# Performance work log

Hardware: AMD Instinct MI355X
Metric: run time of the kernel (lower is better)

## Reference

```python
import jax, jax.numpy as jnp
import numpy as np

B, SEQ = 1, 2048
HEADS, HEAD_DIM = 16, 64
HIDDEN = HEADS * HEAD_DIM          # 1024
EXP = 4
QKVP = HIDDEN * (3 + EXP)          # 7168
VP = HIDDEN * (1 + EXP)            # 5120
DEPTH = 12
EPS = 1e-5
NEG = -1e10


def _alibi_slopes(heads):
    def p2(n):
        start = 2.0 ** (-(2.0 ** (-(np.log2(n) - 3.0))))
        return [start * (start ** i) for i in range(n)]
    if np.log2(heads).is_integer():
        return p2(heads)
    c = 2 ** int(np.floor(np.log2(heads)))
    return p2(c) + p2(2 * c)[0::2][: heads - c]


def _ln(x, g, b):
    m = x.mean(-1, keepdims=True)
    v = ((x - m) ** 2).mean(-1, keepdims=True)
    return (x - m) / jnp.sqrt(v + EPS) * g + b


def setup_inputs():
    key = jax.random.key(0)
    ks = jax.random.split(key, 16)
    init_scale = 2.0 / (DEPTH ** 0.5)
    inp = {
        'x': jax.random.normal(ks[0], (B, SEQ, HIDDEN), jnp.float32),
        'accumulated_logits': 0.02 * jax.random.normal(ks[1], (B, 1, SEQ, SEQ), jnp.float32),
        'in_proj_w': (init_scale / HIDDEN ** 0.5) * jax.random.normal(ks[2], (QKVP, HIDDEN), jnp.float32),
        'out_proj_w': 0.02 * jax.random.normal(ks[3], (HIDDEN, VP), jnp.float32),
        'out_proj_b': 0.02 * jax.random.normal(ks[4], (HIDDEN,), jnp.float32),
        'in_ln_g': 1.0 + 0.02 * jax.random.normal(ks[5], (HIDDEN,), jnp.float32),
        'in_ln_b': 0.02 * jax.random.normal(ks[6], (HIDDEN,), jnp.float32),
        'q_ln_g': 1.0 + 0.02 * jax.random.normal(ks[7], (HIDDEN,), jnp.float32),
        'q_ln_b': 0.02 * jax.random.normal(ks[8], (HIDDEN,), jnp.float32),
        'k_ln_g': 1.0 + 0.02 * jax.random.normal(ks[9], (HIDDEN,), jnp.float32),
        'k_ln_b': 0.02 * jax.random.normal(ks[10], (HIDDEN,), jnp.float32),
        'mid_ln_g': 1.0 + 0.02 * jax.random.normal(ks[11], (HIDDEN * EXP,), jnp.float32),
        'mid_ln_b': 0.02 * jax.random.normal(ks[12], (HIDDEN * EXP,), jnp.float32),
        'out_ln_g': 1.0 + 0.02 * jax.random.normal(ks[13], (HIDDEN,), jnp.float32),
        'out_ln_b': 0.02 * jax.random.normal(ks[14], (HIDDEN,), jnp.float32),
    }
    return inp


def reference(x, accumulated_logits, in_proj_w, out_proj_w, out_proj_b,
              in_ln_g, in_ln_b, q_ln_g, q_ln_b, k_ln_g, k_ln_b,
              mid_ln_g, mid_ln_b, out_ln_g, out_ln_b):
    b, l, d = x.shape
    h = _ln(x, in_ln_g, in_ln_b)
    # Shift: first d//4 channels shifted forward by 1 token (zero-pad front)
    q4 = d // 4
    shifted = jnp.pad(h[:, :, :q4], ((0, 0), (1, 0), (0, 0)))[:, :l]
    h = jnp.concatenate([shifted, h[:, :, q4:]], axis=-1)
    # merged qkvp projection (no bias)
    h = h @ in_proj_w.T                                   # [b, l, qkvp]
    q, k, v, p = jnp.split(h, [HIDDEN, 2 * HIDDEN, 3 * HIDDEN], axis=-1)
    q = _ln(q, q_ln_g, q_ln_b)
    k = _ln(k, k_ln_g, k_ln_b)
    to_heads = lambda t: t.reshape(b, l, HEADS, HEAD_DIM).transpose(0, 2, 1, 3)
    qh, kh, vh = to_heads(q), to_heads(k), to_heads(v)    # [b, h, l, hd]
    logits = jnp.einsum('bhid,bhjd->bhij', qh, kh) * (HEAD_DIM ** -0.5)
    logit_residual = logits.mean(axis=1, keepdims=True)   # [b, 1, l, l]
    idx = jnp.arange(l)
    causal = jnp.where(idx[:, None] >= idx[None, :], 0.0, NEG).astype(x.dtype)
    slopes = jnp.asarray(_alibi_slopes(HEADS), jnp.float32)          # [h]
    alibi = idx.astype(jnp.float32)[None, :] * slopes[:, None]       # [h, j]
    logits = logits + accumulated_logits + alibi[None, :, None, :] + causal[None, None]
    a = jax.nn.softmax(logits, axis=-1)
    o = jnp.einsum('bhij,bhjd->bhid', a, vh)
    o = o.transpose(0, 2, 1, 3).reshape(b, l, HIDDEN)
    p = jax.nn.relu(_ln(p, mid_ln_g, mid_ln_b))
    out = jnp.concatenate([o, p], axis=-1) @ out_proj_w.T + out_proj_b
    out = _ln(out, out_ln_g, out_ln_b)
    return out, logit_residual
```

## Files before the change

### kernel.cpp

```cpp
#include <hip/hip_runtime.h>

#define SEQ 2048
#define HID 1024
#define NHEAD 16
#define HD 64
#define QKVPD 7168
#define VPD 5120
#define NEGV -1e10f

typedef __bf16 bf16;
typedef __attribute__((ext_vector_type(4))) __bf16 bf16x4;
typedef __attribute__((ext_vector_type(8))) __bf16 bf16x8;
typedef __attribute__((ext_vector_type(4))) float f32x4;

#define MFMA16(a, b, c) __builtin_amdgcn_mfma_f32_16x16x32_bf16((a), (b), (c), 0, 0, 0)

#define GLOAD_LDS16(g, l) __builtin_amdgcn_global_load_lds( \
    (const __attribute__((address_space(1))) void*)(g),     \
    (__attribute__((address_space(3))) void*)(l), 16, 0, 0)

__device__ __forceinline__ void reduce2(float& s, float& ss) {
#pragma unroll
  for (int mk = 32; mk >= 1; mk >>= 1) {
    s  += __shfl_xor(s, mk);
    ss += __shfl_xor(ss, mk);
  }
  __shared__ float rtmp[8];
  const int w = threadIdx.x >> 6;
  if ((threadIdx.x & 63) == 0) { rtmp[2 * w] = s; rtmp[2 * w + 1] = ss; }
  __syncthreads();
  s  = rtmp[0] + rtmp[2] + rtmp[4] + rtmp[6];
  ss = rtmp[1] + rtmp[3] + rtmp[5] + rtmp[7];
}

__global__ __launch_bounds__(256) void cvt_f32_bf16(const float* __restrict__ in,
                                                    bf16* __restrict__ out, int n4) {
  int i = blockIdx.x * 256 + threadIdx.x;
  if (i >= n4) return;
  float4 v = ((const float4*)in)[i];
  bf16x4 o = {(bf16)v.x, (bf16)v.y, (bf16)v.z, (bf16)v.w};
  ((bf16x4*)out)[i] = o;
}

__global__ __launch_bounds__(256) void ln_in_shift(const float* __restrict__ x,
                                                   const float* __restrict__ g,
                                                   const float* __restrict__ b,
                                                   bf16* __restrict__ h) {
  const int t = blockIdx.x, tid = threadIdx.x;
  float4 v = ((const float4*)(x + (size_t)t * HID))[tid];
  float s = v.x + v.y + v.z + v.w;
  float ss = v.x * v.x + v.y * v.y + v.z * v.z + v.w * v.w;
  reduce2(s, ss);
  float mean = s * (1.f / HID);
  float var = ss * (1.f / HID) - mean * mean;
  float rstd = rsqrtf(var + 1e-5f);
  int c0 = tid * 4;
  float4 gv = ((const float4*)g)[tid];
  float4 bv = ((const float4*)b)[tid];
  bf16x4 o;
  o[0] = (bf16)((v.x - mean) * rstd * gv.x + bv.x);
  o[1] = (bf16)((v.y - mean) * rstd * gv.y + bv.y);
  o[2] = (bf16)((v.z - mean) * rstd * gv.z + bv.z);
  o[3] = (bf16)((v.w - mean) * rstd * gv.w + bv.w);
  if (c0 >= 256) {
    *(bf16x4*)(h + (size_t)t * HID + c0) = o;
  } else {
    if (t + 1 < SEQ) *(bf16x4*)(h + (size_t)(t + 1) * HID + c0) = o;
    if (t == 0) {
      bf16x4 z = {(bf16)0.f, (bf16)0.f, (bf16)0.f, (bf16)0.f};
      *(bf16x4*)(h + c0) = z;
    }
  }
}

__global__ __launch_bounds__(256) void ln_qk(const bf16* __restrict__ qkvp,
                                             const float* __restrict__ gq, const float* __restrict__ bq,
                                             const float* __restrict__ gk, const float* __restrict__ bk,
                                             bf16* __restrict__ qo, bf16* __restrict__ ko) {
  const int t = blockIdx.x, z = blockIdx.y, tid = threadIdx.x;
  const bf16* in = qkvp + (size_t)t * QKVPD + z * HID;
  bf16* out = (z ? ko : qo) + (size_t)t * HID;
  const float* g = z ? gk : gq;
  const float* bb = z ? bk : bq;
  int c0 = tid * 4;
  bf16x4 iv = *(const bf16x4*)(in + c0);
  float f0 = (float)iv[0], f1 = (float)iv[1], f2 = (float)iv[2], f3 = (float)iv[3];
  float s = f0 + f1 + f2 + f3;
  float ss = f0 * f0 + f1 * f1 + f2 * f2 + f3 * f3;
  reduce2(s, ss);
  float mean = s * (1.f / HID);
  float var = ss * (1.f / HID) - mean * mean;
  float rstd = rsqrtf(var + 1e-5f);
  float4 gv = ((const float4*)g)[tid];
  float4 bv = ((const float4*)bb)[tid];
  bf16x4 o;
  o[0] = (bf16)((f0 - mean) * rstd * gv.x + bv.x);
  o[1] = (bf16)((f1 - mean) * rstd * gv.y + bv.y);
  o[2] = (bf16)((f2 - mean) * rstd * gv.z + bv.z);
  o[3] = (bf16)((f3 - mean) * rstd * gv.w + bv.w);
  *(bf16x4*)(out + c0) = o;
}

__global__ __launch_bounds__(256) void ln_mid(const bf16* __restrict__ qkvp,
                                              const float* __restrict__ g,
                                              const float* __restrict__ b,
                                              bf16* __restrict__ op) {
  const int t = blockIdx.x, tid = threadIdx.x;
  const bf16* in = qkvp + (size_t)t * QKVPD + 3 * HID;
  int c0 = tid * 16;
  bf16x8 a = *(const bf16x8*)(in + c0);
  bf16x8 a2 = *(const bf16x8*)(in + c0 + 8);
  float fv[16];
#pragma unroll
  for (int e = 0; e < 8; ++e) { fv[e] = (float)a[e]; fv[8 + e] = (float)a2[e]; }
  float s = 0.f, ss = 0.f;
#pragma unroll
  for (int e = 0; e < 16; ++e) { s += fv[e]; ss += fv[e] * fv[e]; }
  reduce2(s, ss);
  const float D = 4.f * HID;
  float mean = s / D;
  float var = ss / D - mean * mean;
  float rstd = rsqrtf(var + 1e-5f);
  bf16x8 o1, o2;
#pragma unroll
  for (int q = 0; q < 4; ++q) {
    float4 gv = ((const float4*)g)[tid * 4 + q];
    float4 bv = ((const float4*)b)[tid * 4 + q];
    float r0 = fmaxf(0.f, (fv[q * 4 + 0] - mean) * rstd * gv.x + bv.x);
    float r1 = fmaxf(0.f, (fv[q * 4 + 1] - mean) * rstd * gv.y + bv.y);
    float r2 = fmaxf(0.f, (fv[q * 4 + 2] - mean) * rstd * gv.z + bv.z);
    float r3 = fmaxf(0.f, (fv[q * 4 + 3] - mean) * rstd * gv.w + bv.w);
    if (q < 2) {
      o1[q * 4 + 0] = (bf16)r0; o1[q * 4 + 1] = (bf16)r1;
      o1[q * 4 + 2] = (bf16)r2; o1[q * 4 + 3] = (bf16)r3;
    } else {
      o2[(q - 2) * 4 + 0] = (bf16)r0; o2[(q - 2) * 4 + 1] = (bf16)r1;
      o2[(q - 2) * 4 + 2] = (bf16)r2; o2[(q - 2) * 4 + 3] = (bf16)r3;
    }
  }
  bf16* dst = op + (size_t)t * VPD + HID + c0;
  *(bf16x8*)dst = o1;
  *(bf16x8*)(dst + 8) = o2;
}

__global__ __launch_bounds__(256) void ln_out(const float* __restrict__ cp0,
                                              const float* __restrict__ cp1,
                                              const float* __restrict__ bias,
                                              const float* __restrict__ g,
                                              const float* __restrict__ b,
                                              float* __restrict__ outp) {
  const int t = blockIdx.x, tid = threadIdx.x;
  float4 v  = ((const float4*)(cp0 + (size_t)t * HID))[tid];
  float4 v1 = ((const float4*)(cp1 + (size_t)t * HID))[tid];
  float4 bi = ((const float4*)bias)[tid];
  v.x += v1.x + bi.x; v.y += v1.y + bi.y; v.z += v1.z + bi.z; v.w += v1.w + bi.w;
  float s = v.x + v.y + v.z + v.w;
  float ss = v.x * v.x + v.y * v.y + v.z * v.z + v.w * v.w;
  reduce2(s, ss);
  float mean = s * (1.f / HID);
  float var = ss * (1.f / HID) - mean * mean;
  float rstd = rsqrtf(var + 1e-5f);
  float4 gv = ((const float4*)g)[tid];
  float4 bv = ((const float4*)b)[tid];
  float4 o;
  o.x = (v.x - mean) * rstd * gv.x + bv.x;
  o.y = (v.y - mean) * rstd * gv.y + bv.y;
  o.z = (v.z - mean) * rstd * gv.z + bv.z;
  o.w = (v.w - mean) * rstd * gv.w + bv.w;
  ((float4*)(outp + (size_t)t * HID))[tid] = o;
}

__global__ __launch_bounds__(256) void vtrans(const bf16* __restrict__ qkvp,
                                              bf16* __restrict__ v_t) {
  const int h = blockIdx.y, j0 = blockIdx.x * 64, tid = threadIdx.x;
  __shared__ bf16 tile[64][72];
  int jr = tid >> 2, dcw = (tid & 3) * 16;
  const bf16* src = qkvp + (size_t)(j0 + jr) * QKVPD + 2 * HID + h * HD + dcw;
  bf16x8 a = *(const bf16x8*)src;
  bf16x8 a2 = *(const bf16x8*)(src + 8);
#pragma unroll
  for (int e = 0; e < 8; ++e) { tile[jr][dcw + e] = a[e]; tile[jr][dcw + 8 + e] = a2[e]; }
  __syncthreads();
  int d = tid >> 2, jc = (tid & 3) * 16;
  bf16x8 o1, o2;
#pragma unroll
  for (int e = 0; e < 8; ++e) { o1[e] = tile[jc + e][d]; o2[e] = tile[jc + 8 + e][d]; }
  bf16* dst = v_t + (size_t)(h * HD + d) * SEQ + j0 + jc;
  *(bf16x8*)dst = o1;
  *(bf16x8*)(dst + 8) = o2;
}

template <int OUT_BF16>
__global__ __launch_bounds__(256) void gemm_bt(const bf16* __restrict__ A,
                                               const bf16* __restrict__ B,
                                               void* __restrict__ Cout,
                                               int M, int N, int ld, int kLen,
                                               float scale) {
  __shared__ bf16 As[128 * 32], Bs[128 * 32];
  const int tid = threadIdx.x;
  const int l = tid & 63, w = tid >> 6;
  const int wr = w >> 1, wc = w & 1;
  const int lr = l & 15, lg = l >> 4;
  const int m0 = blockIdx.y * 128, n0 = blockIdx.x * 128;
  const int kBeg = blockIdx.z * kLen, kEnd = kBeg + kLen;

  f32x4 acc[4][4];
#pragma unroll
  for (int i = 0; i < 4; ++i)
#pragma unroll
    for (int j = 0; j < 4; ++j) acc[i][j] = (f32x4){0.f, 0.f, 0.f, 0.f};

  for (int k0 = kBeg; k0 < kEnd; k0 += 32) {
#pragma unroll
    for (int p = 0; p < 2; ++p) {
      int idx = p * 256 + tid;
      int row = idx >> 2, cc = (idx & 3) * 8;
      GLOAD_LDS16(A + (size_t)(m0 + row) * ld + k0 + cc, As + idx * 8);
      GLOAD_LDS16(B + (size_t)(n0 + row) * ld + k0 + cc, Bs + idx * 8);
    }
    __syncthreads();
    bf16x8 af[4], bfr[4];
#pragma unroll
    for (int i = 0; i < 4; ++i) {
      af[i]  = *(const bf16x8*)(As + (wr * 64 + i * 16 + lr) * 32 + lg * 8);
      bfr[i] = *(const bf16x8*)(Bs + (wc * 64 + i * 16 + lr) * 32 + lg * 8);
    }
#pragma unroll
    for (int i = 0; i < 4; ++i)
#pragma unroll
      for (int j = 0; j < 4; ++j) acc[i][j] = MFMA16(af[i], bfr[j], acc[i][j]);
    __syncthreads();
  }

  float* cf = (float*)Cout + (size_t)blockIdx.z * M * N;
#pragma unroll
  for (int i = 0; i < 4; ++i)
#pragma unroll
    for (int j = 0; j < 4; ++j)
#pragma unroll
      for (int r = 0; r < 4; ++r) {
        int rr = m0 + wr * 64 + i * 16 + lg * 4 + r;
        int cc = n0 + wc * 64 + j * 16 + lr;
        if (OUT_BF16)
          ((bf16*)Cout)[(size_t)rr * N + cc] = (bf16)acc[i][j][r];
        else
          cf[(size_t)rr * N + cc] = acc[i][j][r] * scale;
      }
}

__global__ __launch_bounds__(256) void attn_flash(const bf16* __restrict__ q_ln,
                                                  const bf16* __restrict__ k_ln,
                                                  const bf16* __restrict__ v_t,
                                                  const float* __restrict__ acc_lg,
                                                  bf16* __restrict__ o_out) {
  const int head = blockIdx.x;
  const int y = blockIdx.y;
  const int tid = threadIdx.x;
  const int w = tid >> 6, l = tid & 63;
  const int lr = l & 15, lg = l >> 4;
  int R;
  if (w == 0) R = 2 * y; else if (w == 1) R = 2 * y + 1;
  else if (w == 2) R = 126 - 2 * y; else R = 127 - 2 * y;
  const int i0 = R * 16;
  const int hoff = head * HD;
  const float slope = exp2f(-0.5f * (float)(head + 1));

  __shared__ bf16 pbuf[4][16 * 40];
  bf16* pb = pbuf[w];

  bf16x8 qf[2];
#pragma unroll
  for (int kc = 0; kc < 2; ++kc)
    qf[kc] = *(const bf16x8*)(q_ln + (size_t)(i0 + lr) * HID + hoff + kc * 32 + lg * 8);

  f32x4 oacc[4] = {{0.f, 0.f, 0.f, 0.f}, {0.f, 0.f, 0.f, 0.f},
                   {0.f, 0.f, 0.f, 0.f}, {0.f, 0.f, 0.f, 0.f}};
  float mrow[4] = {-3e38f, -3e38f, -3e38f, -3e38f};
  float lsum[4] = {0.f, 0.f, 0.f, 0.f};

  for (int j0 = 0; j0 <= i0 + 15; j0 += 32) {
    f32x4 s[2];
#pragma unroll
    for (int jh = 0; jh < 2; ++jh) {
      f32x4 a = {0.f, 0.f, 0.f, 0.f};
#pragma unroll
      for (int kc = 0; kc < 2; ++kc) {
        bf16x8 kf = *(const bf16x8*)(k_ln + (size_t)(j0 + jh * 16 + lr) * HID +
                                     hoff + kc * 32 + lg * 8);
        a = MFMA16(qf[kc], kf, a);
      }
      s[jh] = a * 0.125f;
    }
    float f[2][4];
#pragma unroll
    for (int jh = 0; jh < 2; ++jh)
#pragma unroll
      for (int r = 0; r < 4; ++r) {
        int i = i0 + lg * 4 + r;
        int j = j0 + jh * 16 + lr;
        f[jh][r] = s[jh][r] + acc_lg[(size_t)i * SEQ + j] + slope * (float)j +
                   ((j <= i) ? 0.f : NEGV);
      }
#pragma unroll
    for (int r = 0; r < 4; ++r) {
      float vm = fmaxf(f[0][r], f[1][r]);
#pragma unroll
      for (int mk = 1; mk < 16; mk <<= 1) vm = fmaxf(vm, __shfl_xor(vm, mk));
      float mnew = fmaxf(mrow[r], vm);
      float scl = __expf(mrow[r] - mnew);
      float p0 = __expf(f[0][r] - mnew);
      float p1 = __expf(f[1][r] - mnew);
      float ps = p0 + p1;
#pragma unroll
      for (int mk = 1; mk < 16; mk <<= 1) ps += __shfl_xor(ps, mk);
      lsum[r] = lsum[r] * scl + ps;
      mrow[r] = mnew;
#pragma unroll
      for (int dc = 0; dc < 4; ++dc) oacc[dc][r] *= scl;
      pb[(lg * 4 + r) * 40 + lr] = (bf16)p0;
      pb[(lg * 4 + r) * 40 + 16 + lr] = (bf16)p1;
    }
    asm volatile("s_waitcnt lgkmcnt(0)" ::: "memory");
    bf16x8 pa = *(const bf16x8*)(pb + lr * 40 + lg * 8);
#pragma unroll
    for (int dc = 0; dc < 4; ++dc) {
      bf16x8 vb = *(const bf16x8*)(v_t + (size_t)(hoff + dc * 16 + lr) * SEQ +
                                   j0 + lg * 8);
      oacc[dc] = MFMA16(pa, vb, oacc[dc]);
    }
  }

#pragma unroll
  for (int dc = 0; dc < 4; ++dc)
#pragma unroll
    for (int r = 0; r < 4; ++r) {
      float o = oacc[dc][r] / lsum[r];
      o_out[(size_t)(i0 + lg * 4 + r) * VPD + hoff + dc * 16 + lr] = (bf16)o;
    }
}

extern "C" void kernel_launch(void* const* d_in, const int* in_sizes, int n_in,
                              void* d_out, int out_size, void* d_ws, size_t ws_size,
                              hipStream_t stream) {
  const float* x      = (const float*)d_in[0];
  const float* acc_lg = (const float*)d_in[1];
  const float* w_in   = (const float*)d_in[2];
  const float* w_out  = (const float*)d_in[3];
  const float* b_out  = (const float*)d_in[4];
  const float* g_in   = (const float*)d_in[5];
  const float* bi_in  = (const float*)d_in[6];
  const float* g_q    = (const float*)d_in[7];
  const float* bi_q   = (const float*)d_in[8];
  const float* g_k    = (const float*)d_in[9];
  const float* bi_k   = (const float*)d_in[10];
  const float* g_mid  = (const float*)d_in[11];
  const float* bi_mid = (const float*)d_in[12];
  const float* g_out  = (const float*)d_in[13];
  const float* bi_o   = (const float*)d_in[14];

  char* ws = (char*)d_ws;
  bf16* h_shift = (bf16*)(ws + 0);
  bf16* wA      = (bf16*)(ws + 4194304);
  bf16* wO      = (bf16*)(ws + 18874368);
  bf16* qkvp    = (bf16*)(ws + 29360128);
  bf16* q_ln    = (bf16*)(ws + 58720256);
  bf16* k_ln    = (bf16*)(ws + 62914560);
  bf16* v_t     = (bf16*)(ws + 67108864);
  bf16* op      = (bf16*)(ws + 71303168);
  float* out_pre = (float*)qkvp;

  float* outp  = (float*)d_out;
  float* resid = outp + (size_t)SEQ * HID;

  cvt_f32_bf16<<<7168, 256, 0, stream>>>(w_in, wA, QKVPD * HID / 4);
  cvt_f32_bf16<<<5120, 256, 0, stream>>>(w_out, wO, HID * VPD / 4);
  ln_in_shift<<<SEQ, 256, 0, stream>>>(x, g_in, bi_in, h_shift);
  gemm_bt<1><<<dim3(QKVPD / 128, SEQ / 128), 256, 0, stream>>>(
      h_shift, wA, qkvp, SEQ, QKVPD, HID, HID, 1.f);
  ln_qk<<<dim3(SEQ, 2), 256, 0, stream>>>(qkvp, g_q, bi_q, g_k, bi_k, q_ln, k_ln);
  ln_mid<<<SEQ, 256, 0, stream>>>(qkvp, g_mid, bi_mid, op);
  vtrans<<<dim3(SEQ / 64, NHEAD), 256, 0, stream>>>(qkvp, v_t);
  gemm_bt<0><<<dim3(SEQ / 128, SEQ / 128), 256, 0, stream>>>(
      q_ln, k_ln, resid, SEQ, SEQ, HID, HID, 1.f / 128.f);
  attn_flash<<<dim3(NHEAD, 32), 256, 0, stream>>>(q_ln, k_ln, v_t, acc_lg, op);
  gemm_bt<0><<<dim3(HID / 128, SEQ / 128, 2), 256, 0, stream>>>(
      op, wO, out_pre, SEQ, HID, VPD, VPD / 2, 1.f);
  ln_out<<<SEQ, 256, 0, stream>>>(out_pre, out_pre + (size_t)SEQ * HID,
                                  b_out, g_out, bi_o, outp);
}
```

Baseline: 396.6 us.

## Restructure flash attention: transposed S, 64-wide KV tiles, exp2 with prescaled Q

```diff
diff --git a/kernel.cpp b/kernel.cpp
--- a/kernel.cpp
+++ b/kernel.cpp
@@ -18,6 +18,8 @@
 #define GLOAD_LDS16(g, l) __builtin_amdgcn_global_load_lds( \
     (const __attribute__((address_space(1))) void*)(g),     \
     (__attribute__((address_space(3))) void*)(l), 16, 0, 0)
+
+#define L2E 1.44269504f
 
 __device__ __forceinline__ void reduce2(float& s, float& ss) {
 #pragma unroll
@@ -82,6 +84,7 @@
   bf16* out = (z ? ko : qo) + (size_t)t * HID;
   const float* g = z ? gk : gq;
   const float* bb = z ? bk : bq;
+  const float osc = z ? 1.0f : 0.125f * L2E;
   int c0 = tid * 4;
   bf16x4 iv = *(const bf16x4*)(in + c0);
   float f0 = (float)iv[0], f1 = (float)iv[1], f2 = (float)iv[2], f3 = (float)iv[3];
@@ -94,10 +97,10 @@
   float4 gv = ((const float4*)g)[tid];
   float4 bv = ((const float4*)bb)[tid];
   bf16x4 o;
-  o[0] = (bf16)((f0 - mean) * rstd * gv.x + bv.x);
-  o[1] = (bf16)((f1 - mean) * rstd * gv.y + bv.y);
-  o[2] = (bf16)((f2 - mean) * rstd * gv.z + bv.z);
-  o[3] = (bf16)((f3 - mean) * rstd * gv.w + bv.w);
+  o[0] = (bf16)(((f0 - mean) * rstd * gv.x + bv.x) * osc);
+  o[1] = (bf16)(((f1 - mean) * rstd * gv.y + bv.y) * osc);
+  o[2] = (bf16)(((f2 - mean) * rstd * gv.z + bv.z) * osc);
+  o[3] = (bf16)(((f3 - mean) * rstd * gv.w + bv.w) * osc);
   *(bf16x4*)(out + c0) = o;
 }
 
@@ -258,15 +261,17 @@
   const int tid = threadIdx.x;
   const int w = tid >> 6, l = tid & 63;
   const int lr = l & 15, lg = l >> 4;
-  int R;
-  if (w == 0) R = 2 * y; else if (w == 1) R = 2 * y + 1;
-  else if (w == 2) R = 126 - 2 * y; else R = 127 - 2 * y;
+  const int role = (w + y) & 3;
+  const int R = role == 0 ? 2 * y : role == 1 ? 2 * y + 1
+              : role == 2 ? 126 - 2 * y : 127 - 2 * y;
   const int i0 = R * 16;
   const int hoff = head * HD;
-  const float slope = exp2f(-0.5f * (float)(head + 1));
-
-  __shared__ bf16 pbuf[4][16 * 40];
-  bf16* pb = pbuf[w];
+  const float slope2 = exp2f(-0.5f * (float)(head + 1)) * L2E;
+
+  __shared__ float bias_s[4][16][68];
+  __shared__ bf16 p_s[4][16][72];
+  float (*bw)[68] = bias_s[w];
+  bf16 (*pw)[72] = p_s[w];
 
   bf16x8 qf[2];
 #pragma unroll
@@ -275,68 +280,108 @@
 
   f32x4 oacc[4] = {{0.f, 0.f, 0.f, 0.f}, {0.f, 0.f, 0.f, 0.f},
                    {0.f, 0.f, 0.f, 0.f}, {0.f, 0.f, 0.f, 0.f}};
-  float mrow[4] = {-3e38f, -3e38f, -3e38f, -3e38f};
-  float lsum[4] = {0.f, 0.f, 0.f, 0.f};
-
-  for (int j0 = 0; j0 <= i0 + 15; j0 += 32) {
-    f32x4 s[2];
-#pragma unroll
-    for (int jh = 0; jh < 2; ++jh) {
+  float mrow = -3e38f, lsum = 0.f;
+  const int iq = i0 + lr;
+
+  for (int j0 = 0; j0 <= i0 + 15; j0 += 64) {
+    bf16x8 kf[4][2];
+#pragma unroll
+    for (int t = 0; t < 4; ++t)
+#pragma unroll
+      for (int kc = 0; kc < 2; ++kc)
+        kf[t][kc] = *(const bf16x8*)(k_ln + (size_t)(j0 + t * 16 + lr) * HID +
+                                     hoff + kc * 32 + lg * 8);
+    bf16x8 vv[4][2];
+#pragma unroll
+    for (int dt = 0; dt < 4; ++dt)
+#pragma unroll
+      for (int c = 0; c < 2; ++c)
+        vv[dt][c] = *(const bf16x8*)(v_t + (size_t)(hoff + dt * 16 + lr) * SEQ +
+                                     j0 + c * 32 + lg * 8);
+    float4 bld[4];
+    {
+      const float* bp = acc_lg + (size_t)(i0 + (l >> 2)) * SEQ + j0 + (l & 3) * 4;
+#pragma unroll
+      for (int qx = 0; qx < 4; ++qx) bld[qx] = *(const float4*)(bp + qx * 16);
+    }
+    f32x4 st[4];
+#pragma unroll
+    for (int t = 0; t < 4; ++t) {
       f32x4 a = {0.f, 0.f, 0.f, 0.f};
-#pragma unroll
-      for (int kc = 0; kc < 2; ++kc) {
-        bf16x8 kf = *(const bf16x8*)(k_ln + (size_t)(j0 + jh * 16 + lr) * HID +
-                                     hoff + kc * 32 + lg * 8);
-        a = MFMA16(qf[kc], kf, a);
+      a = MFMA16(kf[t][0], qf[0], a);
+      a = MFMA16(kf[t][1], qf[1], a);
+      st[t] = a;
+    }
+#pragma unroll
+    for (int qx = 0; qx < 4; ++qx)
+      *(float4*)&bw[l >> 2][(l & 3) * 4 + qx * 16] = bld[qx];
+    asm volatile("s_waitcnt lgkmcnt(0)" ::: "memory");
+    __builtin_amdgcn_sched_barrier(0);
+    const bool diag = (j0 + 64 > i0);
+#pragma unroll
+    for (int t = 0; t < 4; ++t) {
+      f32x4 b4 = *(const f32x4*)&bw[lr][t * 16 + lg * 4];
+      float jt = (float)(j0 + t * 16 + lg * 4);
+#pragma unroll
+      for (int r = 0; r < 4; ++r) {
+        float f = fmaf(b4[r], L2E, st[t][r]);
+        f = fmaf(slope2, jt + (float)r, f);
+        if (diag) {
+          int j = j0 + t * 16 + lg * 4 + r;
+          f = (j <= iq) ? f : -1e30f;
+        }
+        st[t][r] = f;
       }
-      s[jh] = a * 0.125f;
-    }
-    float f[2][4];
-#pragma unroll
-    for (int jh = 0; jh < 2; ++jh)
+    }
+    float pm = st[0][0];
+#pragma unroll
+    for (int t = 0; t < 4; ++t)
+#pragma unroll
+      for (int r = 0; r < 4; ++r) pm = fmaxf(pm, st[t][r]);
+    pm = fmaxf(pm, __shfl_xor(pm, 16));
+    pm = fmaxf(pm, __shfl_xor(pm, 32));
+    float mnew = fmaxf(mrow, pm);
+    float scl = exp2f(mrow - mnew);
+    float ps = 0.f;
+#pragma unroll
+    for (int t = 0; t < 4; ++t)
 #pragma unroll
       for (int r = 0; r < 4; ++r) {
-        int i = i0 + lg * 4 + r;
-        int j = j0 + jh * 16 + lr;
-        f[jh][r] = s[jh][r] + acc_lg[(size_t)i * SEQ + j] + slope * (float)j +
-                   ((j <= i) ? 0.f : NEGV);
+        float p = exp2f(st[t][r] - mnew);
+        st[t][r] = p;
+        ps += p;
       }
-#pragma unroll
-    for (int r = 0; r < 4; ++r) {
-      float vm = fmaxf(f[0][r], f[1][r]);
-#pragma unroll
-      for (int mk = 1; mk < 16; mk <<= 1) vm = fmaxf(vm, __shfl_xor(vm, mk));
-      float mnew = fmaxf(mrow[r], vm);
-      float scl = __expf(mrow[r] - mnew);
-      float p0 = __expf(f[0][r] - mnew);
-      float p1 = __expf(f[1][r] - mnew);
-      float ps = p0 + p1;
-#pragma unroll
-      for (int mk = 1; mk < 16; mk <<= 1) ps += __shfl_xor(ps, mk);
-      lsum[r] = lsum[r] * scl + ps;
-      mrow[r] = mnew;
-#pragma unroll
-      for (int dc = 0; dc < 4; ++dc) oacc[dc][r] *= scl;
-      pb[(lg * 4 + r) * 40 + lr] = (bf16)p0;
-      pb[(lg * 4 + r) * 40 + 16 + lr] = (bf16)p1;
+    ps += __shfl_xor(ps, 16);
+    ps += __shfl_xor(ps, 32);
+    lsum = lsum * scl + ps;
+    mrow = mnew;
+#pragma unroll
+    for (int dt = 0; dt < 4; ++dt) oacc[dt] *= scl;
+#pragma unroll
+    for (int t = 0; t < 4; ++t) {
+      bf16x4 pk = {(bf16)st[t][0], (bf16)st[t][1], (bf16)st[t][2], (bf16)st[t][3]};
+      *(bf16x4*)&pw[lr][t * 16 + lg * 4] = pk;
     }
     asm volatile("s_waitcnt lgkmcnt(0)" ::: "memory");
-    bf16x8 pa = *(const bf16x8*)(pb + lr * 40 + lg * 8);
-#pragma unroll
-    for (int dc = 0; dc < 4; ++dc) {
-      bf16x8 vb = *(const bf16x8*)(v_t + (size_t)(hoff + dc * 16 + lr) * SEQ +
-                                   j0 + lg * 8);
-      oacc[dc] = MFMA16(pa, vb, oacc[dc]);
-    }
-  }
-
-#pragma unroll
-  for (int dc = 0; dc < 4; ++dc)
-#pragma unroll
-    for (int r = 0; r < 4; ++r) {
-      float o = oacc[dc][r] / lsum[r];
-      o_out[(size_t)(i0 + lg * 4 + r) * VPD + hoff + dc * 16 + lr] = (bf16)o;
-    }
+    __builtin_amdgcn_sched_barrier(0);
+    bf16x8 pf[2];
+#pragma unroll
+    for (int c = 0; c < 2; ++c)
+      pf[c] = *(const bf16x8*)&pw[lr][c * 32 + lg * 8];
+#pragma unroll
+    for (int dt = 0; dt < 4; ++dt)
+#pragma unroll
+      for (int c = 0; c < 2; ++c)
+        oacc[dt] = MFMA16(vv[dt][c], pf[c], oacc[dt]);
+  }
+
+  const float rl = 1.f / lsum;
+#pragma unroll
+  for (int dt = 0; dt < 4; ++dt) {
+    bf16x4 ov = {(bf16)(oacc[dt][0] * rl), (bf16)(oacc[dt][1] * rl),
+                 (bf16)(oacc[dt][2] * rl), (bf16)(oacc[dt][3] * rl)};
+    *(bf16x4*)(o_out + (size_t)(i0 + lr) * VPD + hoff + dt * 16 + lg * 4) = ov;
+  }
 }
 
 extern "C" void kernel_launch(void* const* d_in, const int* in_sizes, int n_in,
@@ -381,7 +426,7 @@
   ln_mid<<<SEQ, 256, 0, stream>>>(qkvp, g_mid, bi_mid, op);
   vtrans<<<dim3(SEQ / 64, NHEAD), 256, 0, stream>>>(qkvp, v_t);
   gemm_bt<0><<<dim3(SEQ / 128, SEQ / 128), 256, 0, stream>>>(
-      q_ln, k_ln, resid, SEQ, SEQ, HID, HID, 1.f / 128.f);
+      q_ln, k_ln, resid, SEQ, SEQ, HID, HID, 1.f / (16.f * L2E));
   attn_flash<<<dim3(NHEAD, 32), 256, 0, stream>>>(q_ln, k_ln, v_t, acc_lg, op);
   gemm_bt<0><<<dim3(HID / 128, SEQ / 128, 2), 256, 0, stream>>>(
       op, wO, out_pre, SEQ, HID, VPD, VPD / 2, 1.f);
```

Measured after the change: 375.9 us. 5.2% less time.
